# Optimization experiments

Measured on AMD Instinct MI355X. Metric: run time of the kernel, lower is better.

The kernel has to match this reference:

```python
import jax, jax.numpy as jnp
import numpy as np

BSZ, SEQ, HID = 4, 4096, 2048
NUM_EXPERTS, TOPK = 64, 8


def setup_inputs() -> dict:
    key = jax.random.key(0)
    kx, kw = jax.random.split(key)
    x = jax.random.normal(kx, (BSZ, SEQ, HID), dtype=jnp.float32)
    # nn.Linear default init scale ~ 1/sqrt(fan_in); exact init irrelevant for correctness baseline
    W = jax.random.normal(kw, (NUM_EXPERTS, HID), dtype=jnp.float32) * (HID ** -0.5)
    b = jnp.zeros((NUM_EXPERTS,), dtype=jnp.float32)
    return {"x": x, "W": W, "b": b}


def reference(x, W, b):
    # gate: (bsz, seq, num_experts)
    gate = jnp.einsum("bsh,eh->bse", x, W) + b
    # top-k along expert dim
    logits, ids = jax.lax.top_k(gate, TOPK)  # (bsz, seq, topk)
    # scatter top-k logits into a -inf mask, then softmax over all experts
    bsz, seq, ne = gate.shape
    bi = jnp.arange(bsz)[:, None, None]
    si = jnp.arange(seq)[None, :, None]
    mask = jnp.full(gate.shape, -jnp.inf, dtype=gate.dtype)
    mask = mask.at[bi, si, ids].set(logits)
    probs = jax.nn.softmax(mask, axis=-1)  # zeros outside top-k
    return (probs, ids)
```

## Files before the change

kernel.cpp:

```cpp
#include <hip/hip_runtime.h>
#include <math.h>

#define BSZ 4
#define SEQ 4096
#define HID 2048
#define NE 64
#define TOPK 8
#define NTOK (BSZ*SEQ)
#define NSPLIT 4
#define KSPL (HID/NSPLIT)
#define KC 64
#define BT 128

#define XS 66
#define WSTR 68

__global__ __launch_bounds__(256, 2)
void moe_gate_gemm(const float* __restrict__ x, const float* __restrict__ W,
                   float* __restrict__ part) {
    __shared__ __align__(16) float xlds[BT * XS];
    __shared__ __align__(16) float wlds[KC * WSTR];

    const int tid   = threadIdx.x;
    const int tile  = blockIdx.x;
    const int split = blockIdx.y;
    const int T0 = tile * BT;
    const int k0 = split * KSPL;

    const int tx = tid & 15;
    const int ty = tid >> 4;

    double acc[8][4];
    #pragma unroll
    for (int i = 0; i < 8; i++)
        #pragma unroll
        for (int j = 0; j < 4; j++) acc[i][j] = 0.0;

    for (int c = 0; c < KSPL / KC; c++) {
        const int kc = k0 + c * KC;

        {
            const int jt = tid >> 4;
            const int j4 = tid & 15;
            #pragma unroll
            for (int r = 0; r < 8; r++) {
                const int t = jt + r * 16;
                const float4 v = *reinterpret_cast<const float4*>(
                    &x[(size_t)(T0 + t) * HID + kc + j4 * 4]);
                float2* p = reinterpret_cast<float2*>(&xlds[t * XS + j4 * 4]);
                p[0] = make_float2(v.x, v.y);
                p[1] = make_float2(v.z, v.w);
            }
        }
        {
            const int e = tid >> 2;
            const int q = tid & 3;
            #pragma unroll
            for (int r = 0; r < 4; r++) {
                const int k4 = q + r * 4;
                const float4 v = *reinterpret_cast<const float4*>(
                    &W[(size_t)e * HID + kc + k4 * 4]);
                wlds[(k4 * 4 + 0) * WSTR + e] = v.x;
                wlds[(k4 * 4 + 1) * WSTR + e] = v.y;
                wlds[(k4 * 4 + 2) * WSTR + e] = v.z;
                wlds[(k4 * 4 + 3) * WSTR + e] = v.w;
            }
        }
        __syncthreads();

        #pragma unroll 4
        for (int k = 0; k < KC; k++) {
            const float4 wv = *reinterpret_cast<const float4*>(&wlds[k * WSTR + tx * 4]);
            float xv[8];
            #pragma unroll
            for (int i = 0; i < 8; i++) xv[i] = xlds[(ty * 8 + i) * XS + k];
            #pragma unroll
            for (int i = 0; i < 8; i++) {
                acc[i][0] += (double)xv[i] * (double)wv.x;
                acc[i][1] += (double)xv[i] * (double)wv.y;
                acc[i][2] += (double)xv[i] * (double)wv.z;
                acc[i][3] += (double)xv[i] * (double)wv.w;
            }
        }
        __syncthreads();
    }

    #pragma unroll
    for (int i = 0; i < 8; i++) {
        const int tok = T0 + ty * 8 + i;
        const float4 v = make_float4((float)acc[i][0], (float)acc[i][1],
                                     (float)acc[i][2], (float)acc[i][3]);
        *reinterpret_cast<float4*>(
            &part[((size_t)split * NTOK + tok) * NE + tx * 4]) = v;
    }
}

__global__ __launch_bounds__(256)
void moe_topk_softmax(const float* __restrict__ part, const float* __restrict__ b,
                      float* __restrict__ probs, float* __restrict__ ids) {
    const int lane  = threadIdx.x & 63;
    const int w     = threadIdx.x >> 6;
    const int token = blockIdx.x * 4 + w;

    float g = b[lane];
    #pragma unroll
    for (int s = 0; s < NSPLIT; s++)
        g += part[((size_t)s * NTOK + token) * NE + lane];

    const float gorig = g;
    float cur = g;
    float m = 0.f, denom = 0.f;
    int   myid = 0;
    bool  sel = false;

    #pragma unroll
    for (int it = 0; it < TOPK; it++) {
        float v = cur;
        int idx = lane;
        #pragma unroll
        for (int d = 1; d < 64; d <<= 1) {
            const float ov = __shfl_xor(v, d, 64);
            const int   oi = __shfl_xor(idx, d, 64);
            if (ov > v || (ov == v && oi < idx)) { v = ov; idx = oi; }
        }
        if (it == 0) m = v;
        denom += expf(v - m);
        if (lane == idx) { sel = true; cur = -INFINITY; }
        if (lane == it)  myid = idx;
    }

    probs[(size_t)token * NE + lane] = sel ? expf(gorig - m) / denom : 0.f;
    if (lane < TOPK) ids[(size_t)token * TOPK + lane] = (float)myid;
}

extern "C" void kernel_launch(void* const* d_in, const int* in_sizes, int n_in,
                              void* d_out, int out_size, void* d_ws, size_t ws_size,
                              hipStream_t stream) {
    const float* x = (const float*)d_in[0];
    const float* W = (const float*)d_in[1];
    const float* b = (const float*)d_in[2];

    float* probs = (float*)d_out;
    float* ids   = (float*)d_out + (size_t)NTOK * NE;
    float* part  = (float*)d_ws;

    dim3 g1(NTOK / BT, NSPLIT);
    moe_gate_gemm<<<g1, 256, 0, stream>>>(x, W, part);
    moe_topk_softmax<<<NTOK / 4, 256, 0, stream>>>(part, b, probs, ids);
}
```

Baseline: 282.9 us.

## Shrink token tile to 64, transpose x in LDS, raise occupancy

Halves the token tile to 64 rows per block and gives each thread a 4x4 double-precision accumulator block in place of 8x4. x is now stored transposed in LDS, so the inner loop reads x and W as float4 vectors rather than eight scalar loads. Launch bounds ask for four blocks per CU instead of two, trading register reuse for more occupancy and a larger grid. The FP64 FMA count per token is unchanged, while W is reloaded from global memory for twice as many blocks.

```diff
diff --git a/kernel.cpp b/kernel.cpp
--- a/kernel.cpp
+++ b/kernel.cpp
@@ -10,16 +10,16 @@
 #define NSPLIT 4
 #define KSPL (HID/NSPLIT)
 #define KC 64
-#define BT 128
+#define BT 64
 
-#define XS 66
-#define WSTR 68
+#define XS 68
+#define WSS 68
 
-__global__ __launch_bounds__(256, 2)
+__global__ __launch_bounds__(256, 4)
 void moe_gate_gemm(const float* __restrict__ x, const float* __restrict__ W,
                    float* __restrict__ part) {
-    __shared__ __align__(16) float xlds[BT * XS];
-    __shared__ __align__(16) float wlds[KC * WSTR];
+    __shared__ __align__(16) float xlds[KC * XS];
+    __shared__ __align__(16) float wlds[KC * WSS];
 
     const int tid   = threadIdx.x;
     const int tile  = blockIdx.x;
@@ -30,64 +30,54 @@
     const int tx = tid & 15;
     const int ty = tid >> 4;
 
-    double acc[8][4];
+    const int row = tid & 63;
+    const int q   = tid >> 6;
+
+    double acc[4][4];
     #pragma unroll
-    for (int i = 0; i < 8; i++)
+    for (int i = 0; i < 4; i++)
         #pragma unroll
         for (int j = 0; j < 4; j++) acc[i][j] = 0.0;
 
     for (int c = 0; c < KSPL / KC; c++) {
         const int kc = k0 + c * KC;
 
-        {
-            const int jt = tid >> 4;
-            const int j4 = tid & 15;
-            #pragma unroll
-            for (int r = 0; r < 8; r++) {
-                const int t = jt + r * 16;
-                const float4 v = *reinterpret_cast<const float4*>(
-                    &x[(size_t)(T0 + t) * HID + kc + j4 * 4]);
-                float2* p = reinterpret_cast<float2*>(&xlds[t * XS + j4 * 4]);
-                p[0] = make_float2(v.x, v.y);
-                p[1] = make_float2(v.z, v.w);
-            }
-        }
-        {
-            const int e = tid >> 2;
-            const int q = tid & 3;
-            #pragma unroll
-            for (int r = 0; r < 4; r++) {
-                const int k4 = q + r * 4;
-                const float4 v = *reinterpret_cast<const float4*>(
-                    &W[(size_t)e * HID + kc + k4 * 4]);
-                wlds[(k4 * 4 + 0) * WSTR + e] = v.x;
-                wlds[(k4 * 4 + 1) * WSTR + e] = v.y;
-                wlds[(k4 * 4 + 2) * WSTR + e] = v.z;
-                wlds[(k4 * 4 + 3) * WSTR + e] = v.w;
-            }
+        #pragma unroll
+        for (int r = 0; r < 4; r++) {
+            const int k4 = r * 4 + q;
+            const float4 xv = *reinterpret_cast<const float4*>(
+                &x[(size_t)(T0 + row) * HID + kc + k4 * 4]);
+            xlds[(k4 * 4 + 0) * XS + row] = xv.x;
+            xlds[(k4 * 4 + 1) * XS + row] = xv.y;
+            xlds[(k4 * 4 + 2) * XS + row] = xv.z;
+            xlds[(k4 * 4 + 3) * XS + row] = xv.w;
+            const float4 wv = *reinterpret_cast<const float4*>(
+                &W[(size_t)row * HID + kc + k4 * 4]);
+            wlds[(k4 * 4 + 0) * WSS + row] = wv.x;
+            wlds[(k4 * 4 + 1) * WSS + row] = wv.y;
+            wlds[(k4 * 4 + 2) * WSS + row] = wv.z;
+            wlds[(k4 * 4 + 3) * WSS + row] = wv.w;
         }
         __syncthreads();
 
         #pragma unroll 4
         for (int k = 0; k < KC; k++) {
-            const float4 wv = *reinterpret_cast<const float4*>(&wlds[k * WSTR + tx * 4]);
-            float xv[8];
+            const float4 xv = *reinterpret_cast<const float4*>(&xlds[k * XS + ty * 4]);
+            const float4 wv = *reinterpret_cast<const float4*>(&wlds[k * WSS + tx * 4]);
+            const float xr[4] = {xv.x, xv.y, xv.z, xv.w};
+            const float wr[4] = {wv.x, wv.y, wv.z, wv.w};
             #pragma unroll
-            for (int i = 0; i < 8; i++) xv[i] = xlds[(ty * 8 + i) * XS + k];
-            #pragma unroll
-            for (int i = 0; i < 8; i++) {
-                acc[i][0] += (double)xv[i] * (double)wv.x;
-                acc[i][1] += (double)xv[i] * (double)wv.y;
-                acc[i][2] += (double)xv[i] * (double)wv.z;
-                acc[i][3] += (double)xv[i] * (double)wv.w;
-            }
+            for (int i = 0; i < 4; i++)
+                #pragma unroll
+                for (int j = 0; j < 4; j++)
+                    acc[i][j] += (double)xr[i] * (double)wr[j];
         }
         __syncthreads();
     }
 
     #pragma unroll
-    for (int i = 0; i < 8; i++) {
-        const int tok = T0 + ty * 8 + i;
+    for (int i = 0; i < 4; i++) {
+        const int tok = T0 + ty * 4 + i;
         const float4 v = make_float4((float)acc[i][0], (float)acc[i][1],
                                      (float)acc[i][2], (float)acc[i][3]);
         *reinterpret_cast<float4*>(
```

Result: no change. 280.1 us (-1.0%).
